# Optimization experiments

Measured on AMD Instinct MI355X. Metric: run time of the kernel, lower is better.

Reference implementation:

```python
import jax, jax.numpy as jnp
import numpy as np

N_NODES = 100000
N_EDGES = 3200000
N_GRAPHS = 128
HIDDEN = 128
DEPTH = 3


def setup_inputs() -> dict:
    key = jax.random.key(0)
    ks = jax.random.split(key, 12)
    x = jax.random.normal(ks[0], (N_NODES, 1), dtype=jnp.float32)
    edge_index = jax.random.randint(ks[1], (2, N_EDGES), 0, N_NODES, dtype=jnp.int64)
    batch = jnp.sort(jax.random.randint(ks[2], (N_NODES,), 0, N_GRAPHS, dtype=jnp.int64))
    s = 1.0 / np.sqrt(HIDDEN)
    return {
        "x": x,
        "edge_index": edge_index,
        "batch": batch,
        "W_emb": jax.random.normal(ks[3], (1, HIDDEN), dtype=jnp.float32),
        "b_emb": jax.random.normal(ks[4], (HIDDEN,), dtype=jnp.float32) * 0.01,
        "W_gnn": jax.random.normal(ks[5], (DEPTH, HIDDEN, HIDDEN), dtype=jnp.float32) * s,
        "b_gnn": jax.random.normal(ks[6], (DEPTH, HIDDEN), dtype=jnp.float32) * 0.01,
        "W_c1": jax.random.normal(ks[7], (HIDDEN, HIDDEN // 2), dtype=jnp.float32) * s,
        "b_c1": jax.random.normal(ks[8], (HIDDEN // 2,), dtype=jnp.float32) * 0.01,
        "W_c2": jax.random.normal(ks[9], (HIDDEN // 2, 1), dtype=jnp.float32) * s,
        "b_c2": jax.random.normal(ks[10], (1,), dtype=jnp.float32) * 0.01,
    }


def reference(x, edge_index, batch, W_emb, b_emb, W_gnn, b_gnn, W_c1, b_c1, W_c2, b_c2):
    # --- GCN normalization (self-loops + symmetric deg^-1/2) ---
    loop = jnp.arange(N_NODES, dtype=edge_index.dtype)
    row = jnp.concatenate([edge_index[0], loop])  # source nodes
    col = jnp.concatenate([edge_index[1], loop])  # target nodes
    deg = jax.ops.segment_sum(jnp.ones_like(col, dtype=jnp.float32), col, num_segments=N_NODES)
    dinv = jnp.where(deg > 0, jax.lax.rsqrt(jnp.maximum(deg, 1.0)), 0.0)
    norm = dinv[row] * dinv[col]  # [E+N]

    # --- node embedding ---
    h = x @ W_emb + b_emb  # [N, H]

    # --- GCN layers: linear -> gather -> normalize -> scatter-add -> bias -> relu ---
    for l in range(DEPTH):
        h_lin = h @ W_gnn[l]                       # [N, H]
        msgs = h_lin[row] * norm[:, None]          # [E+N, H]
        agg = jax.ops.segment_sum(msgs, col, num_segments=N_NODES)
        h = jax.nn.relu(agg + b_gnn[l])

    # --- global mean pool per graph ---
    counts = jax.ops.segment_sum(jnp.ones((N_NODES,), jnp.float32), batch, num_segments=N_GRAPHS)
    sums = jax.ops.segment_sum(h, batch, num_segments=N_GRAPHS)
    g = sums / jnp.maximum(counts, 1.0)[:, None]   # [G, H]

    # --- classifier (dropout is identity in eval) ---
    z = jax.nn.relu(g @ W_c1 + b_c1)
    out = jax.nn.sigmoid(z @ W_c2 + b_c2)          # [G, 1]
    return out.squeeze(-1)                          # [G]
```

## Files before the change

### kernel.cpp

```cpp
#include <hip/hip_runtime.h>
#include <math.h>

#define HID 128
#define CAP 96
#define TILE 8192
#define WSH 9
#define BUKCAP 24576

typedef unsigned int uint;
typedef unsigned short ushort;
typedef float f32x2 __attribute__((ext_vector_type(2)));
typedef float f32x4 __attribute__((ext_vector_type(4)));
typedef short bf16x8 __attribute__((ext_vector_type(8)));

__device__ inline ushort f2bf(float f) {
    uint u = __float_as_uint(f);
    return (ushort)((u + 0x7fffu + ((u >> 16) & 1u)) >> 16);
}
__device__ inline float bflo(uint u) { return __uint_as_float(u << 16); }
__device__ inline float bfhi(uint u) { return __uint_as_float(u & 0xffff0000u); }
__device__ inline uint packbf(float a, float b) {
    return (uint)f2bf(a) | ((uint)f2bf(b) << 16);
}
__device__ inline bf16x8 as_bf16x8(uint4 u) {
    union { uint4 a; bf16x8 b; } c;
    c.a = u;
    return c.b;
}

__device__ inline f32x2 fp8lo(uint q) { return __builtin_amdgcn_cvt_pk_f32_fp8(q, false); }
__device__ inline f32x2 fp8hi(uint q) { return __builtin_amdgcn_cvt_pk_f32_fp8(q, true); }
__device__ inline uint pack4fp8(float a, float b, float c, float d) {
    int t = __builtin_amdgcn_cvt_pk_fp8_f32(a, b, 0, false);
    return (uint)__builtin_amdgcn_cvt_pk_fp8_f32(c, d, t, true);
}


__global__ void __launch_bounds__(256) k_part(const int* __restrict__ row,
                                              const int* __restrict__ col,
                                              int* __restrict__ bukCur,
                                              uint* __restrict__ recs, int E) {
    __shared__ int hist[256];
    __shared__ int hist2[256];
    __shared__ uint base[256];
    int t = threadIdx.x;
    hist[t] = 0;
    hist2[t] = 0;
    __syncthreads();
    int i0 = blockIdx.x * TILE;
    int i1 = min(E, i0 + TILE);
    for (int i = i0 + t; i < i1; i += 256) {
        int b = col[i] >> WSH;
        atomicAdd(&hist[b], 1);
    }
    __syncthreads();
    if (hist[t] > 0) base[t] = (uint)atomicAdd(&bukCur[t], hist[t]);
    __syncthreads();
    for (int i = i0 + t; i < i1; i += 256) {
        int c = col[i];
        int b = c >> WSH;
        uint p = (uint)atomicAdd(&hist2[b], 1);
        uint idx = base[b] + p;
        if (idx < BUKCAP)
            recs[(size_t)b * BUKCAP + idx] = (uint)row[i] | ((uint)(c & 511) << 17);
    }
}

__global__ void __launch_bounds__(256) k_fbin(const uint* __restrict__ recs,
                                              const int* __restrict__ bukCur,
                                              int* __restrict__ cnt,
                                              int* __restrict__ ebin, int N) {
    __shared__ int lcnt[512];
    int b = blockIdx.x;
    int t = threadIdx.x;
    lcnt[t] = 0;
    lcnt[t + 256] = 0;
    __syncthreads();
    int n = min(bukCur[b], BUKCAP);
    const uint* rp = recs + (size_t)b * BUKCAP;
    int cbase = b << WSH;
    for (int j = t; j < n; j += 256) {
        uint u = rp[j];
        int r = (int)(u & 0x1FFFFu);
        int cl = (int)(u >> 17);
        int p = atomicAdd(&lcnt[cl], 1);
        if (p < CAP) ebin[(size_t)(cbase + cl) * CAP + p] = r;
    }
    __syncthreads();
    int c0 = cbase + t;
    if (c0 < N) cnt[c0] = lcnt[t];
    int c1 = cbase + t + 256;
    if (c1 < N) cnt[c1] = lcnt[t + 256];
}

__global__ void k_prep(const int* __restrict__ cnt, const float* __restrict__ x,
                       float* __restrict__ dinv, float2* __restrict__ pk0, int N) {
    int i = blockIdx.x * blockDim.x + threadIdx.x;
    if (i < N) {
        float d = rsqrtf((float)cnt[i] + 1.0f);
        dinv[i] = d;
        pk0[i] = make_float2(d, d * x[i]);
    }
}


__global__ void k_uv(const float* __restrict__ W_emb, const float* __restrict__ b_emb,
                     const float* __restrict__ W0, float* __restrict__ u, float* __restrict__ v) {
    int j = threadIdx.x;
    float su = 0.f, sv = 0.f;
    for (int k = 0; k < HID; ++k) {
        float w = W0[k * HID + j];
        su = fmaf(W_emb[k], w, su);
        sv = fmaf(b_emb[k], w, sv);
    }
    u[j] = su;
    v[j] = sv;
}

__global__ void k_sagg(const int* __restrict__ cnt, const int* __restrict__ ebin,
                       const float* __restrict__ x, const float* __restrict__ dinv,
                       const float2* __restrict__ pk0,
                       float* __restrict__ s0, float* __restrict__ s1, int N) {
    int c = blockIdx.x * blockDim.x + threadIdx.x;
    if (c >= N) return;
    float dc = dinv[c];
    float A = 0.f, B = 0.f;
    int n = min(cnt[c], CAP);
    const int* bp = ebin + (size_t)c * CAP;
    int k = 0;
    for (; k + 4 <= n; k += 4) {
        float2 p0 = pk0[bp[k]], p1 = pk0[bp[k + 1]];
        float2 p2 = pk0[bp[k + 2]], p3 = pk0[bp[k + 3]];
        A += (p0.x + p1.x) + (p2.x + p3.x);
        B += (p0.y + p1.y) + (p2.y + p3.y);
    }
    for (; k < n; ++k) {
        float2 p = pk0[bp[k]];
        A += p.x;
        B += p.y;
    }
    float d2 = dc * dc;
    s0[c] = fmaf(dc, A, d2);
    s1[c] = fmaf(dc, B, d2 * x[c]);
}

__global__ void k_h1(const float* __restrict__ s0, const float* __restrict__ s1,
                     const float* __restrict__ u, const float* __restrict__ v,
                     const float* __restrict__ b0, const float* __restrict__ dinv,
                     uint* __restrict__ g8, int total) {
    int idx = blockIdx.x * blockDim.x + threadIdx.x;
    if (idx >= total) return;
    int c = idx >> 5, j = (idx & 31) * 4;
    float t0 = s1[c], t1 = s0[c];
    float dc = dinv[c];
    float v0 = fmaxf(fmaf(t0, u[j + 0], fmaf(t1, v[j + 0], b0[j + 0])), 0.f);
    float v1 = fmaxf(fmaf(t0, u[j + 1], fmaf(t1, v[j + 1], b0[j + 1])), 0.f);
    float v2 = fmaxf(fmaf(t0, u[j + 2], fmaf(t1, v[j + 2], b0[j + 2])), 0.f);
    float v3 = fmaxf(fmaf(t0, u[j + 3], fmaf(t1, v[j + 3], b0[j + 3])), 0.f);
    g8[idx] = pack4fp8(dc * v0, dc * v1, dc * v2, dc * v3);
}


__global__ void __launch_bounds__(256) k_agg(const int* __restrict__ cnt,
                                             const int* __restrict__ ebin,
                                             const float* __restrict__ dinv,
                                             const uint* __restrict__ g8,
                                             uint* __restrict__ a, int N) {
    int wave = (blockIdx.x * 256 + threadIdx.x) >> 6;
    int lane = threadIdx.x & 63;
    if (wave >= N) return;
    int c = wave;
    int sl = lane & 31;
    int halfid = lane >> 5;
    bool h0 = (halfid == 0);

    f32x2 acc01, acc23;
    {
        uint sq = g8[c * 32 + sl];
        f32x2 lo = fp8lo(sq), hi = fp8hi(sq);
        f32x2 z = {0.f, 0.f};
        acc01 = h0 ? lo : z;
        acc23 = h0 ? hi : z;
    }

    int n = min(cnt[c], CAP);
    const int* __restrict__ bp = ebin + (size_t)c * CAP;
    for (int base = 0; base < n; base += 64) {
        int cw = min(n - base, 64);
        int r = 0;
        if (lane < cw) r = bp[base + lane];
        int j = 0;
        for (; j + 8 <= cw; j += 8) {
            int rA = __shfl(r, j + halfid);
            int rB = __shfl(r, j + 2 + halfid);
            int rC = __shfl(r, j + 4 + halfid);
            int rD = __shfl(r, j + 6 + halfid);
            uint qA = g8[rA * 32 + sl];
            uint qB = g8[rB * 32 + sl];
            uint qC = g8[rC * 32 + sl];
            uint qD = g8[rD * 32 + sl];
            acc01 += fp8lo(qA); acc23 += fp8hi(qA);
            acc01 += fp8lo(qB); acc23 += fp8hi(qB);
            acc01 += fp8lo(qC); acc23 += fp8hi(qC);
            acc01 += fp8lo(qD); acc23 += fp8hi(qD);
        }
        for (; j + 2 <= cw; j += 2) {
            int rA = __shfl(r, j + halfid);
            uint qA = g8[rA * 32 + sl];
            acc01 += fp8lo(qA); acc23 += fp8hi(qA);
        }
        if (j < cw) {
            int rA = __shfl(r, j);
            uint qA = g8[rA * 32 + sl];
            if (h0) { acc01 += fp8lo(qA); acc23 += fp8hi(qA); }
        }
    }

    float a0 = acc01.x, a1 = acc01.y, a2 = acc23.x, a3 = acc23.y;
    a0 += __shfl_xor(a0, 32);
    a1 += __shfl_xor(a1, 32);
    a2 += __shfl_xor(a2, 32);
    a3 += __shfl_xor(a3, 32);
    if (h0) {
        float dc = dinv[c];
        uint2 o;
        o.x = packbf(dc * a0, dc * a1);
        o.y = packbf(dc * a2, dc * a3);
        ((uint2*)(a + (size_t)c * 64))[sl] = o;
    }
}


__global__ void k_wfrag(const float* __restrict__ W_gnn, uint4* __restrict__ wfrag) {
    int gid = blockIdx.x * 256 + threadIdx.x;
    if (gid >= 4096) return;
    int l = gid >> 11;
    int rem = gid & 2047;
    int kb = rem >> 9;
    int nt = (rem >> 6) & 7;
    int lane = rem & 63;
    int k0 = kb * 32 + (lane >> 4) * 8;
    int n = nt * 16 + (lane & 15);
    const float* Wp = W_gnn + (size_t)(l + 1) * HID * HID;
    uint4 o;
    o.x = packbf(Wp[(k0 + 0) * HID + n], Wp[(k0 + 1) * HID + n]);
    o.y = packbf(Wp[(k0 + 2) * HID + n], Wp[(k0 + 3) * HID + n]);
    o.z = packbf(Wp[(k0 + 4) * HID + n], Wp[(k0 + 5) * HID + n]);
    o.w = packbf(Wp[(k0 + 6) * HID + n], Wp[(k0 + 7) * HID + n]);
    wfrag[gid] = o;
}

#define RCH 32
__global__ void __launch_bounds__(256, 2) k_gemm(const uint* __restrict__ A,
                                                 const uint4* __restrict__ wfrag,
                                                 const float* __restrict__ bias,
                                                 const float* __restrict__ rowscale,
                                                 uint* __restrict__ H8, int N) {
    __shared__ uint4 sAf[4][2][64];
    __shared__ float sEp[4][16][68];
    int t = threadIdx.x;
    int w = t >> 6;
    int lane = t & 63;
    int rowgrp = w >> 1;
    int colh = w & 1;

    bf16x8 Bf[4][4];
#pragma unroll
    for (int kb = 0; kb < 4; ++kb)
#pragma unroll
        for (int i = 0; i < 4; ++i)
            Bf[kb][i] = as_bf16x8(wfrag[(kb * 8 + colh * 4 + i) * 64 + lane]);

    float4 bb = ((const float4*)bias)[colh * 16 + (lane & 15)];

    int nchunk = (N + RCH - 1) / RCH;
    for (int ch = blockIdx.x; ch < nchunk; ch += gridDim.x) {
        int r0 = ch * RCH;
        __syncthreads();
#pragma unroll
        for (int s = 0; s < 2; ++s) {
            int i = t + s * 256;
            int kb = i >> 7;
            int rg = (i >> 6) & 1;
            int ln = i & 63;
            int gr = r0 + rg * 16 + (ln & 15);
            gr = min(gr, N - 1);
            sAf[kb][rg][ln] = ((const uint4*)(A + (size_t)gr * 64))[kb * 4 + (ln >> 4)];
        }
        __syncthreads();

        f32x4 acc[4] = {{0.f, 0.f, 0.f, 0.f}, {0.f, 0.f, 0.f, 0.f},
                        {0.f, 0.f, 0.f, 0.f}, {0.f, 0.f, 0.f, 0.f}};
#pragma unroll
        for (int kb = 0; kb < 4; ++kb) {
            bf16x8 af = as_bf16x8(sAf[kb][rowgrp][lane]);
#pragma unroll
            for (int i = 0; i < 4; ++i)
                acc[i] = __builtin_amdgcn_mfma_f32_16x16x32_bf16(af, Bf[kb][i], acc[i], 0, 0, 0);
        }

#pragma unroll
        for (int i = 0; i < 4; ++i) {
#pragma unroll
            for (int reg = 0; reg < 4; ++reg)
                sEp[w][(lane >> 4) * 4 + reg][i * 16 + (lane & 15)] = acc[i][reg];
        }
#pragma unroll
        for (int e = 0; e < 4; ++e) {
            int rr = (lane >> 4) + 4 * e;
            int cu = lane & 15;
            const float* sp = &sEp[w][rr][cu * 4];
            int rowg = r0 + rowgrp * 16 + rr;
            if (rowg < N) {
                float sc = rowscale ? rowscale[rowg] : 1.0f;
                float o0 = sc * fmaxf(sp[0] + bb.x, 0.f);
                float o1 = sc * fmaxf(sp[1] + bb.y, 0.f);
                float o2 = sc * fmaxf(sp[2] + bb.z, 0.f);
                float o3 = sc * fmaxf(sp[3] + bb.w, 0.f);
                H8[(size_t)rowg * 32 + colh * 16 + cu] = pack4fp8(o0, o1, o2, o3);
            }
        }
    }
}


__global__ void k_pool(const uint* __restrict__ h8, const int* __restrict__ batch,
                       float* __restrict__ gpool, float* __restrict__ gcnt, int N) {
    int gi = blockIdx.x >> 2, part = blockIdx.x & 3;
    int t = threadIdx.x;
    int ui = t & 31;
    int sub = t >> 5;
    int lo = 0, hi = N;
    while (lo < hi) { int m = (lo + hi) >> 1; if (batch[m] < gi) lo = m + 1; else hi = m; }
    int start = lo;
    lo = start; hi = N;
    while (lo < hi) { int m = (lo + hi) >> 1; if (batch[m] <= gi) lo = m + 1; else hi = m; }
    int end = lo;
    if (part == 0 && t == 0) gcnt[gi] = (float)(end - start);
    int len = end - start;
    int q = (len + 15) >> 4;
    int seg = part * 4 + sub;
    int rs = start + seg * q;
    int re = min(end, rs + q);
    float s0 = 0.f, s1 = 0.f, s2 = 0.f, s3 = 0.f;
    for (int i = rs; i < re; ++i) {
        uint qq = h8[(size_t)i * 32 + ui];
        f32x2 lo2 = fp8lo(qq), hi2 = fp8hi(qq);
        s0 += lo2.x; s1 += lo2.y; s2 += hi2.x; s3 += hi2.y;
    }
    if (re > rs) {
        float* gp = gpool + gi * HID + ui * 4;
        atomicAdd(gp + 0, s0);
        atomicAdd(gp + 1, s1);
        atomicAdd(gp + 2, s2);
        atomicAdd(gp + 3, s3);
    }
}

__global__ void k_cls(const float* __restrict__ gpool, const float* __restrict__ gcnt,
                      const float* __restrict__ Wc1, const float* __restrict__ bc1,
                      const float* __restrict__ Wc2, const float* __restrict__ bc2,
                      float* __restrict__ out) {
    int g = blockIdx.x;
    int j = threadIdx.x;
    float inv = 1.0f / fmaxf(gcnt[g], 1.0f);
    float z = bc1[j];
    for (int k = 0; k < HID; ++k) z = fmaf(gpool[g * HID + k] * inv, Wc1[k * 64 + j], z);
    z = fmaxf(z, 0.f);
    float p = z * Wc2[j];
    for (int off = 32; off; off >>= 1) p += __shfl_down(p, off);
    if (j == 0) out[g] = 1.0f / (1.0f + expf(-(p + bc2[0])));
}


extern "C" void kernel_launch(void* const* d_in, const int* in_sizes, int n_in,
                              void* d_out, int out_size, void* d_ws, size_t ws_size,
                              hipStream_t stream) {
    const float* x     = (const float*)d_in[0];
    const int*   eidx  = (const int*)d_in[1];
    const int*   batch = (const int*)d_in[2];
    const float* W_emb = (const float*)d_in[3];
    const float* b_emb = (const float*)d_in[4];
    const float* W_gnn = (const float*)d_in[5];
    const float* b_gnn = (const float*)d_in[6];
    const float* W_c1  = (const float*)d_in[7];
    const float* b_c1  = (const float*)d_in[8];
    const float* W_c2  = (const float*)d_in[9];
    const float* b_c2  = (const float*)d_in[10];

    const int N = in_sizes[0];
    const int E = in_sizes[1] / 2;
    const int G = out_size;
    const int* row = eidx;
    const int* col = eidx + E;
    const int NBUK = (N + 511) >> WSH;

    char* ws = (char*)d_ws;
    auto alloc = [&](size_t bytes) -> void* {
        void* p = (void*)ws;
        ws += (bytes + 255) & ~(size_t)255;
        return p;
    };
    int*    cnt    = (int*)alloc((size_t)N * 4);
    float*  dinv   = (float*)alloc((size_t)N * 4);
    float2* pk0    = (float2*)alloc((size_t)N * 8);
    int*    bukCur = (int*)alloc(256 * 4);
    uint*   recs   = (uint*)alloc((size_t)NBUK * BUKCAP * 4);
    int*    ebin   = (int*)alloc((size_t)N * CAP * 4);
    float*  s0     = (float*)alloc((size_t)N * 4);
    float*  s1     = (float*)alloc((size_t)N * 4);
    float*  u      = (float*)alloc(HID * 4);
    float*  v      = (float*)alloc(HID * 4);
    uint*   G8     = (uint*)alloc((size_t)N * 32 * 4);
    uint*   A      = (uint*)alloc((size_t)N * 64 * 4);
    uint4*  wfrag  = (uint4*)alloc(4096 * 16);
    float*  gpool  = (float*)alloc((size_t)G * HID * 4);
    float*  gcnt   = (float*)alloc((size_t)G * 4);

    hipMemsetAsync(bukCur, 0, 256 * 4, stream);
    hipMemsetAsync(gpool, 0, (size_t)G * HID * 4, stream);

    k_part<<<(E + TILE - 1) / TILE, 256, 0, stream>>>(row, col, bukCur, recs, E);
    k_fbin<<<NBUK, 256, 0, stream>>>(recs, bukCur, cnt, ebin, N);
    k_prep<<<(N + 255) / 256, 256, 0, stream>>>(cnt, x, dinv, pk0, N);

    k_uv<<<1, HID, 0, stream>>>(W_emb, b_emb, W_gnn, u, v);
    k_sagg<<<(N + 255) / 256, 256, 0, stream>>>(cnt, ebin, x, dinv, pk0, s0, s1, N);
    k_h1<<<(N * 32 + 255) / 256, 256, 0, stream>>>(s0, s1, u, v, b_gnn, dinv, G8, N * 32);

    k_wfrag<<<16, 256, 0, stream>>>(W_gnn, wfrag);

    int nchunk = (N + RCH - 1) / RCH;
    int gblk = nchunk < 768 ? nchunk : 768;
    for (int l = 1; l < 3; ++l) {
        k_agg<<<(N + 3) / 4, 256, 0, stream>>>(cnt, ebin, dinv, G8, A, N);
        k_gemm<<<gblk, 256, 0, stream>>>(A, wfrag + (size_t)(l - 1) * 2048,
                                         b_gnn + (size_t)l * HID,
                                         (l == 1) ? dinv : (const float*)nullptr,
                                         G8, N);
    }

    k_pool<<<G * 4, 128, 0, stream>>>(G8, batch, gpool, gcnt, N);
    k_cls<<<G, 64, 0, stream>>>(gpool, gcnt, W_c1, b_c1, W_c2, b_c2, (float*)d_out);
}
```

Before: 381.0 us.

## Stage partition tiles in LDS, pre-scale edge indices, deepen gather unroll

The partition kernel now reads each tile's col and row arrays from global memory once into shared memory, so the second pass no longer re-reads them. The tile size drops so the staging buffers fit in LDS and more blocks are launched. Edge bins now store source indices pre-multiplied by 32, which removes the per-edge multiply in the fp8 aggregation gather; the float2 aggregation undoes this with a shift. The gather loop is also unrolled to eight loads in flight per iteration to raise memory-level parallelism. The cost is more LDS per block and higher register use.

```diff
diff --git a/kernel.cpp b/kernel.cpp
--- a/kernel.cpp
+++ b/kernel.cpp
@@ -3,7 +3,7 @@
 
 #define HID 128
 #define CAP 96
-#define TILE 8192
+#define TILE 2048
 #define WSH 9
 #define BUKCAP 24576
 
@@ -17,8 +17,6 @@
     uint u = __float_as_uint(f);
     return (ushort)((u + 0x7fffu + ((u >> 16) & 1u)) >> 16);
 }
-__device__ inline float bflo(uint u) { return __uint_as_float(u << 16); }
-__device__ inline float bfhi(uint u) { return __uint_as_float(u & 0xffff0000u); }
 __device__ inline uint packbf(float a, float b) {
     return (uint)f2bf(a) | ((uint)f2bf(b) << 16);
 }
@@ -43,26 +41,31 @@
     __shared__ int hist[256];
     __shared__ int hist2[256];
     __shared__ uint base[256];
+    __shared__ int scol[TILE];
+    __shared__ int srow[TILE];
     int t = threadIdx.x;
     hist[t] = 0;
     hist2[t] = 0;
     __syncthreads();
     int i0 = blockIdx.x * TILE;
-    int i1 = min(E, i0 + TILE);
-    for (int i = i0 + t; i < i1; i += 256) {
-        int b = col[i] >> WSH;
-        atomicAdd(&hist[b], 1);
+    int nrem = min(TILE, E - i0);
+    for (int k = t; k < nrem; k += 256) {
+        int c = col[i0 + k];
+        int r = row[i0 + k];
+        scol[k] = c;
+        srow[k] = r;
+        atomicAdd(&hist[c >> WSH], 1);
     }
     __syncthreads();
     if (hist[t] > 0) base[t] = (uint)atomicAdd(&bukCur[t], hist[t]);
     __syncthreads();
-    for (int i = i0 + t; i < i1; i += 256) {
-        int c = col[i];
+    for (int k = t; k < nrem; k += 256) {
+        int c = scol[k];
         int b = c >> WSH;
         uint p = (uint)atomicAdd(&hist2[b], 1);
         uint idx = base[b] + p;
         if (idx < BUKCAP)
-            recs[(size_t)b * BUKCAP + idx] = (uint)row[i] | ((uint)(c & 511) << 17);
+            recs[(size_t)b * BUKCAP + idx] = (uint)srow[k] | ((uint)(c & 511) << 17);
     }
 }
 
@@ -84,7 +87,7 @@
         int r = (int)(u & 0x1FFFFu);
         int cl = (int)(u >> 17);
         int p = atomicAdd(&lcnt[cl], 1);
-        if (p < CAP) ebin[(size_t)(cbase + cl) * CAP + p] = r;
+        if (p < CAP) ebin[(size_t)(cbase + cl) * CAP + p] = r << 5;
     }
     __syncthreads();
     int c0 = cbase + t;
@@ -129,13 +132,13 @@
     const int* bp = ebin + (size_t)c * CAP;
     int k = 0;
     for (; k + 4 <= n; k += 4) {
-        float2 p0 = pk0[bp[k]], p1 = pk0[bp[k + 1]];
-        float2 p2 = pk0[bp[k + 2]], p3 = pk0[bp[k + 3]];
+        float2 p0 = pk0[bp[k] >> 5], p1 = pk0[bp[k + 1] >> 5];
+        float2 p2 = pk0[bp[k + 2] >> 5], p3 = pk0[bp[k + 3] >> 5];
         A += (p0.x + p1.x) + (p2.x + p3.x);
         B += (p0.y + p1.y) + (p2.y + p3.y);
     }
     for (; k < n; ++k) {
-        float2 p = pk0[bp[k]];
+        float2 p = pk0[bp[k] >> 5];
         A += p.x;
         B += p.y;
     }
@@ -187,31 +190,44 @@
     const int* __restrict__ bp = ebin + (size_t)c * CAP;
     for (int base = 0; base < n; base += 64) {
         int cw = min(n - base, 64);
-        int r = 0;
-        if (lane < cw) r = bp[base + lane];
+        int ro = 0;
+        if (lane < cw) ro = bp[base + lane];
+        int pairs = cw >> 1;
         int j = 0;
-        for (; j + 8 <= cw; j += 8) {
-            int rA = __shfl(r, j + halfid);
-            int rB = __shfl(r, j + 2 + halfid);
-            int rC = __shfl(r, j + 4 + halfid);
-            int rD = __shfl(r, j + 6 + halfid);
-            uint qA = g8[rA * 32 + sl];
-            uint qB = g8[rB * 32 + sl];
-            uint qC = g8[rC * 32 + sl];
-            uint qD = g8[rD * 32 + sl];
+        for (; j + 8 <= pairs; j += 8) {
+            int oA = __shfl(ro, 2 * j + halfid);
+            int oB = __shfl(ro, 2 * j + 2 + halfid);
+            int oC = __shfl(ro, 2 * j + 4 + halfid);
+            int oD = __shfl(ro, 2 * j + 6 + halfid);
+            int oE = __shfl(ro, 2 * j + 8 + halfid);
+            int oF = __shfl(ro, 2 * j + 10 + halfid);
+            int oG = __shfl(ro, 2 * j + 12 + halfid);
+            int oH = __shfl(ro, 2 * j + 14 + halfid);
+            uint qA = g8[oA + sl];
+            uint qB = g8[oB + sl];
+            uint qC = g8[oC + sl];
+            uint qD = g8[oD + sl];
+            uint qE = g8[oE + sl];
+            uint qF = g8[oF + sl];
+            uint qG = g8[oG + sl];
+            uint qH = g8[oH + sl];
             acc01 += fp8lo(qA); acc23 += fp8hi(qA);
             acc01 += fp8lo(qB); acc23 += fp8hi(qB);
             acc01 += fp8lo(qC); acc23 += fp8hi(qC);
             acc01 += fp8lo(qD); acc23 += fp8hi(qD);
-        }
-        for (; j + 2 <= cw; j += 2) {
-            int rA = __shfl(r, j + halfid);
-            uint qA = g8[rA * 32 + sl];
+            acc01 += fp8lo(qE); acc23 += fp8hi(qE);
+            acc01 += fp8lo(qF); acc23 += fp8hi(qF);
+            acc01 += fp8lo(qG); acc23 += fp8hi(qG);
+            acc01 += fp8lo(qH); acc23 += fp8hi(qH);
+        }
+        for (; j < pairs; ++j) {
+            int oA = __shfl(ro, 2 * j + halfid);
+            uint qA = g8[oA + sl];
             acc01 += fp8lo(qA); acc23 += fp8hi(qA);
         }
-        if (j < cw) {
-            int rA = __shfl(r, j);
-            uint qA = g8[rA * 32 + sl];
+        if (cw & 1) {
+            int oA = __shfl(ro, cw - 1);
+            uint qA = g8[oA + sl];
             if (h0) { acc01 += fp8lo(qA); acc23 += fp8hi(qA); }
         }
     }
```

Result: slower. 389.5 us (+2.2%).
